# Optimization experiments

Hardware: AMD Instinct MI355X
Metric: run time of the kernel (lower is better)

The kernel has to match this reference:

```python
import jax, jax.numpy as jnp
import numpy as np

B = 8192
K = 40          # history blocks of 61
STATS = 383     # 99 base + 120 + 10 + 150 + 4 option dims
D = 165 + 61 * K + STATS  # 2988


def _mha(q, k, v, kpm, w_in, b_in, w_out, b_out, nh=4):
    """PyTorch nn.MultiheadAttention (batch_first) math. kpm: True = masked key."""
    Bq, Lq, E = q.shape
    hd = E // nh
    wq, wk, wv = jnp.split(w_in, 3, axis=0)
    bq, bk, bv = jnp.split(b_in, 3)
    qh = (q @ wq.T + bq).reshape(Bq, Lq, nh, hd).transpose(0, 2, 1, 3)
    kh = (k @ wk.T + bk).reshape(Bq, -1, nh, hd).transpose(0, 2, 1, 3)
    vh = (v @ wv.T + bv).reshape(Bq, -1, nh, hd).transpose(0, 2, 1, 3)
    s = jnp.einsum('bhqd,bhkd->bhqk', qh, kh) * jnp.float32(1.0 / np.sqrt(hd))
    if kpm is not None:
        s = jnp.where(kpm[:, None, None, :], jnp.float32(-1e9), s)
    a = jax.nn.softmax(s, axis=-1)
    o = jnp.einsum('bhqk,bhkd->bhqd', a, vh).transpose(0, 2, 1, 3).reshape(Bq, Lq, E)
    return o @ w_out.T + b_out


def _ln(x, g, b, eps=1e-5):
    m = x.mean(-1, keepdims=True)
    v = ((x - m) ** 2).mean(-1, keepdims=True)
    return (x - m) / jnp.sqrt(v + eps) * g + b


def setup_inputs() -> dict:
    key = jax.random.key(0)
    ks = iter(jax.random.split(key, 64))
    def p(shape, scale=0.02):
        return jax.random.normal(next(ks), shape, dtype=jnp.float32) * scale
    return {
        'obs': jax.random.normal(next(ks), (B, D), dtype=jnp.float32),
        'seat_team_vec': jax.random.normal(next(ks), (B, 6), dtype=jnp.float32),
        'card_emb': p((40, 32)),
        'w_cnt_hand': p((16, 3)), 'b_cnt_hand': p((16,)),
        'w_cnt_cap': p((16, 2)), 'b_cnt_cap': p((16,)),
        'h2t_win': p((96, 32)), 'h2t_bin': p((96,)), 'h2t_wout': p((32, 32)), 'h2t_bout': p((32,)),
        't2h_win': p((96, 32)), 't2h_bin': p((96,)), 't2h_wout': p((32, 32)), 't2h_bout': p((32,)),
        'w_merge': p((64, 224)), 'b_merge': p((64,)),
        'w_hproj': p((64, 61)), 'b_hproj': p((64,)),
        'pos_emb': p((40, 64)),
        'enc_win': p((192, 64)), 'enc_bin': p((192,)), 'enc_wout': p((64, 64)), 'enc_bout': p((64,)),
        'ln1_g': jnp.ones((64,), jnp.float32), 'ln1_b': jnp.zeros((64,), jnp.float32),
        'w_ff1': p((128, 64)), 'b_ff1': p((128,)),
        'w_ff2': p((64, 128)), 'b_ff2': p((64,)),
        'ln2_g': jnp.ones((64,), jnp.float32), 'ln2_b': jnp.zeros((64,), jnp.float32),
        'w_stats': p((64, STATS)), 'b_stats': p((64,)),
        'w_seat': p((32, 6)), 'b_seat': p((32,)),
        'w_comb': p((256, 224)), 'b_comb': p((256,)),
    }


def reference(obs, seat_team_vec, card_emb, w_cnt_hand, b_cnt_hand, w_cnt_cap, b_cnt_cap,
              h2t_win, h2t_bin, h2t_wout, h2t_bout, t2h_win, t2h_bin, t2h_wout, t2h_bout,
              w_merge, b_merge, w_hproj, b_hproj, pos_emb,
              enc_win, enc_bin, enc_wout, enc_bout, ln1_g, ln1_b,
              w_ff1, b_ff1, w_ff2, b_ff2, ln2_g, ln2_b,
              w_stats, b_stats, w_seat, b_seat, w_comb, b_comb):
    Bn = obs.shape[0]
    k = K  # static: decoded from D = 165 + 61*K + STATS
    hand_table = obs[:, :83]
    captured = obs[:, 83:165]
    history = obs[:, 165:165 + 61 * k]
    stats = obs[:, 165 + 61 * k:]

    hand_mask = hand_table[:, :40]
    other_counts = hand_table[:, 40:43]
    table_mask = hand_table[:, 43:83]

    hand_feat = hand_mask @ card_emb      # [B,32]
    table_feat = table_mask @ card_emb
    other_cnt_feat = jax.nn.relu(other_counts @ w_cnt_hand.T + b_cnt_hand)

    hand_present = hand_mask > 0.5
    table_present = table_mask > 0.5
    hand_seq = hand_mask[:, :, None] * card_emb    # [B,40,32]
    table_seq = table_mask[:, :, None] * card_emb

    # _safe_mha: rows whose keys are all padded produce zeros
    h2t = _mha(hand_seq, table_seq, table_seq, ~table_present, h2t_win, h2t_bin, h2t_wout, h2t_bout)
    h2t = jnp.where(table_present.any(axis=1)[:, None, None], h2t, jnp.float32(0.0))
    t2h = _mha(table_seq, hand_seq, hand_seq, ~hand_present, t2h_win, t2h_bin, t2h_wout, t2h_bout)
    t2h = jnp.where(hand_present.any(axis=1)[:, None, None], t2h, jnp.float32(0.0))

    def masked_mean(x, present):
        m = present[:, :, None].astype(x.dtype)
        return (x * m).sum(1) / jnp.maximum(m.sum(1), 1.0)
    hand_attn_feat = masked_mean(h2t, hand_present)
    table_attn_feat = masked_mean(t2h, table_present)

    cap0_feat = captured[:, :40] @ card_emb
    cap1_feat = captured[:, 40:80] @ card_emb
    cap_cnt_feat = jax.nn.relu(captured[:, 80:82] @ w_cnt_cap.T + b_cnt_cap)

    set_merged = jnp.concatenate([hand_feat, table_feat, cap0_feat, cap1_feat,
                                  hand_attn_feat, table_attn_feat,
                                  other_cnt_feat, cap_cnt_feat], axis=1)  # [B,224]
    set_feat = jax.nn.relu(set_merged @ w_merge.T + b_merge)              # [B,64]

    # 1-layer post-norm TransformerEncoder (eval mode, no dropout)
    hseq = history.reshape(Bn, k, 61) @ w_hproj.T + b_hproj + pos_emb[:k]  # [B,k,64]
    sa = _mha(hseq, hseq, hseq, None, enc_win, enc_bin, enc_wout, enc_bout)
    x = _ln(hseq + sa, ln1_g, ln1_b)
    ff = jax.nn.relu(x @ w_ff1.T + b_ff1) @ w_ff2.T + b_ff2
    x = _ln(x + ff, ln2_g, ln2_b)
    hist_feat = x.mean(axis=1)                                            # [B,64]

    stats_feat = jax.nn.relu(stats @ w_stats.T + b_stats)                 # [B,64]
    seat_feat = jax.nn.relu(seat_team_vec @ w_seat.T + b_seat)            # [B,32]

    combined = jnp.concatenate([set_feat, hist_feat, stats_feat, seat_feat], axis=1)  # [B,224]
    return jax.nn.relu(combined @ w_comb.T + b_comb)                      # [B,256]
```

## Files before the change

### kernel.cpp

```cpp
#include <hip/hip_runtime.h>

#define TPB 512

#define OFF_PE      0
#define OFF_HPROJ   7680
#define OFF_POSB    11584
#define OFF_FRAG    14144
#define FR_QKV      0
#define FR_OUT      12288
#define FR_FF1      16384
#define FR_FF2      24576
#define OFF_MERGE   46912
#define OFF_STATS   61248
#define OFF_COMB    85760
#define OFF_H2TWO   143104
#define OFF_T2HWO   144128
#define WS_TOTAL    145152

#define SA_OFF   0
#define SB_OFF   10240
#define SC_OFF   20480
#define QT_OFF   30720
#define FFH_OFF  10240
#define FFL_OFF  23296
#define AH_OFF   36352
#define AL_OFF   43264
#define SHT_OFF  50176
#define SOM_OFF  50840
#define SSM_OFF  51096
#define SCB_OFF  51992
#define SCNT_OFF 53016
#define SMEM_BYTES 53024

typedef __attribute__((ext_vector_type(8))) short bf16x8;
typedef __attribute__((ext_vector_type(4))) float f32x4;

struct P {
  const float *obs, *seat, *ce, *wch, *bch, *wcc, *bcc,
    *h2t_win, *h2t_bin, *h2t_wout, *h2t_bout,
    *t2h_win, *t2h_bin, *t2h_wout, *t2h_bout,
    *w_merge, *b_merge, *w_hproj, *b_hproj, *pos,
    *enc_win, *enc_bin, *enc_wout, *enc_bout,
    *ln1_g, *ln1_b, *w_ff1, *b_ff1, *w_ff2, *b_ff2, *ln2_g, *ln2_b,
    *w_stats, *b_stats, *w_seat, *b_seat, *w_comb, *b_comb;
  const float* ws;
  float* out;
};

__device__ __host__ inline unsigned bfpack(float a, float b, int plane) {
  unsigned ua = __float_as_uint(a) & 0xFFFF0000u;
  unsigned ub = __float_as_uint(b) & 0xFFFF0000u;
  if (plane == 0) return (ua >> 16) | ub;
  float ra = a - __uint_as_float(ua), rb = b - __uint_as_float(ub);
  return (__float_as_uint(ra) >> 16) | (__float_as_uint(rb) & 0xFFFF0000u);
}

__device__ inline void split_pair(float a, float b, unsigned& hi, unsigned& lo) {
  unsigned ua = __float_as_uint(a) & 0xFFFF0000u;
  unsigned ub = __float_as_uint(b) & 0xFFFF0000u;
  hi = (ua >> 16) | ub;
  float ra = a - __uint_as_float(ua), rb = b - __uint_as_float(ub);
  lo = (__float_as_uint(ra) >> 16) | (__float_as_uint(rb) & 0xFFFF0000u);
}

__global__ void prep_kernel(P p, float* ws) {
  int t = blockIdx.x * blockDim.x + threadIdx.x;
  if (t >= WS_TOTAL) return;
  if (t < OFF_HPROJ) {
    int arr = t / 1280, rem = t - arr * 1280;
    int i = rem >> 5, d = rem & 31;
    const float* win = (arr < 3) ? p.h2t_win : p.t2h_win;
    const float* wr = win + ((arr % 3) * 32 + d) * 32;
    const float* cr = p.ce + i * 32;
    float acc = 0.f;
    #pragma unroll
    for (int j = 0; j < 32; ++j) acc += cr[j] * wr[j];
    ws[t] = acc;
  } else if (t < OFF_POSB) {
    int r = t - OFF_HPROJ; int j = r >> 6, d = r & 63;
    ws[t] = p.w_hproj[d * 61 + j];
  } else if (t < OFF_FRAG) {
    int r = t - OFF_POSB; int d = r & 63;
    ws[t] = p.b_hproj[d] + p.pos[r];
  } else if (t < OFF_MERGE) {
    int r = t - OFF_FRAG;
    int plane, kt, nt, lane, u;
    const float* src; int ldk;
    if (r < FR_OUT) {
      plane = r / 6144; r %= 6144; kt = r / 3072; r %= 3072;
      nt = r >> 8; r &= 255; lane = r >> 2; u = r & 3;
      src = p.enc_win; ldk = 64;
    } else if (r < FR_FF1) {
      r -= FR_OUT; plane = r >> 11; r &= 2047; kt = r >> 10; r &= 1023;
      nt = r >> 8; r &= 255; lane = r >> 2; u = r & 3;
      src = p.enc_wout; ldk = 64;
    } else if (r < FR_FF2) {
      r -= FR_FF1; plane = r >> 12; r &= 4095; kt = r >> 11; r &= 2047;
      nt = r >> 8; r &= 255; lane = r >> 2; u = r & 3;
      src = p.w_ff1; ldk = 64;
    } else {
      r -= FR_FF2; plane = r >> 12; r &= 4095; kt = r >> 10; r &= 1023;
      nt = r >> 8; r &= 255; lane = r >> 2; u = r & 3;
      src = p.w_ff2; ldk = 128;
    }
    int k = kt * 32 + (lane >> 4) * 8 + u * 2;
    int n = nt * 16 + (lane & 15);
    float a = src[n * ldk + k], b = src[n * ldk + k + 1];
    ((unsigned*)ws)[t] = bfpack(a, b, plane);
  } else if (t < OFF_STATS) {
    int r = t - OFF_MERGE; int j = r >> 6, d = r & 63;
    ws[t] = p.w_merge[d * 224 + j];
  } else if (t < OFF_COMB) {
    int r = t - OFF_STATS; int j = r >> 6, d = r & 63;
    ws[t] = p.w_stats[d * 383 + j];
  } else if (t < OFF_H2TWO) {
    int r = t - OFF_COMB; int j = r >> 8, d = r & 255;
    ws[t] = p.w_comb[d * 224 + j];
  } else if (t < OFF_T2HWO) {
    int r = t - OFF_H2TWO; int e = r >> 5, d = r & 31;
    ws[t] = p.h2t_wout[d * 32 + e];
  } else {
    int r = t - OFF_T2HWO; int e = r >> 5, d = r & 31;
    ws[t] = p.t2h_wout[d * 32 + e];
  }
}

#define FMA4(acc, a4, w0, w1, w2, w3)                                   \
  acc.x += a4.x * w0.x + a4.y * w1.x + a4.z * w2.x + a4.w * w3.x;       \
  acc.y += a4.x * w0.y + a4.y * w1.y + a4.z * w2.y + a4.w * w3.y;       \
  acc.z += a4.x * w0.z + a4.y * w1.z + a4.z * w2.z + a4.w * w3.z;       \
  acc.w += a4.x * w0.w + a4.y * w1.w + a4.z * w2.w + a4.w * w3.w;

__global__ __launch_bounds__(TPB, 3) void enc_row(P p) {
  const int row = blockIdx.x;
  const int tid = threadIdx.x;
  const int lane = tid & 63, wq = tid >> 6;
  const int lane15 = lane & 15, lg = lane >> 4;

  __shared__ unsigned smem_u[SMEM_BYTES / 4];
  char* smem = (char*)smem_u;
  float* sA   = (float*)(smem + SA_OFF);
  float* sB   = (float*)(smem + SB_OFF);
  float* sC   = (float*)(smem + SC_OFF);
  float* s_ht = (float*)(smem + SHT_OFF);
  float* s_om = (float*)(smem + SOM_OFF);
  float* s_sm = (float*)(smem + SSM_OFF);
  float* s_cb = (float*)(smem + SCB_OFF);
  int*   s_cnt = (int*)(smem + SCNT_OFF);

  const float* orow = p.obs + (size_t)row * 2988;
  const float* ws = p.ws;
  const unsigned* wsu = (const unsigned*)ws;

  if (tid < 165) s_ht[tid] = orow[tid];
  if (tid < 32) {
    float a = 0.f;
    for (int i = 0; i < 40; ++i) a += orow[i] * p.ce[i * 32 + tid];
    s_sm[tid] = a;
  } else if (tid < 64) {
    int d = tid - 32; float a = 0.f;
    for (int i = 0; i < 40; ++i) a += orow[43 + i] * p.ce[i * 32 + d];
    s_sm[32 + d] = a;
  } else if (tid < 96) {
    int d = tid - 64; float a = 0.f;
    for (int i = 0; i < 40; ++i) a += orow[83 + i] * p.ce[i * 32 + d];
    s_sm[64 + d] = a;
  } else if (tid < 128) {
    int d = tid - 96; float a = 0.f;
    for (int i = 0; i < 40; ++i) a += orow[123 + i] * p.ce[i * 32 + d];
    s_sm[96 + d] = a;
  } else if (tid < 144) {
    int d = tid - 128;
    float a = p.bch[d];
    for (int j = 0; j < 3; ++j) a += orow[40 + j] * p.wch[d * 3 + j];
    s_sm[192 + d] = fmaxf(a, 0.f);
  } else if (tid < 160) {
    int d = tid - 144;
    float a = p.bcc[d];
    for (int j = 0; j < 2; ++j) a += orow[163 + j] * p.wcc[d * 2 + j];
    s_sm[208 + d] = fmaxf(a, 0.f);
  }
  if (tid >= 192 && tid < 256) s_om[tid - 192] = 0.f;
  if (tid >= 256 && tid < 320) s_cb[128 + tid - 256] = p.b_stats[tid - 256];
  if (tid >= 384 && tid < 448) s_cb[tid - 384] = p.b_merge[tid - 384];
  if (tid == 320) {
    int c = 0; for (int i = 0; i < 40; ++i) c += (orow[i] > 0.5f);
    s_cnt[0] = c;
  } else if (tid == 321) {
    int c = 0; for (int i = 0; i < 40; ++i) c += (orow[43 + i] > 0.5f);
    s_cnt[1] = c;
  }
  if (tid >= 448) {
    int z = tid - 448;
    unsigned* zh = (unsigned*)(smem + AH_OFF + 40 * 144);
    unsigned* zl = (unsigned*)(smem + AL_OFF + 40 * 144);
    for (int m = z; m < 288; m += 64) { zh[m] = 0u; zl[m] = 0u; }
  }
  __syncthreads();
  #define OB(i) s_ht[i]

  for (int t = tid; t < 736; t += TPB) {
    if (t < 320) {
      int d0 = (t & 15) << 2, i0 = (t >> 4) << 1;
      const float* wt = ws + OFF_HPROJ + d0;
      float4 acc0 = *(const float4*)(ws + OFF_POSB + (i0 + 0) * 64 + d0);
      float4 acc1 = *(const float4*)(ws + OFF_POSB + (i0 + 1) * 64 + d0);
      const float* h0 = orow + 165 + (i0 + 0) * 61;
      const float* h1 = orow + 165 + (i0 + 1) * 61;
      for (int j = 0; j < 61; ++j) {
        float4 w = *(const float4*)(wt + j * 64);
        float a0 = h0[j], a1 = h1[j];
        acc0.x += a0 * w.x; acc0.y += a0 * w.y; acc0.z += a0 * w.z; acc0.w += a0 * w.w;
        acc1.x += a1 * w.x; acc1.y += a1 * w.y; acc1.z += a1 * w.z; acc1.w += a1 * w.w;
      }
      *(float4*)(sA + (i0 + 0) * 64 + d0) = acc0;
      *(float4*)(sA + (i0 + 1) * 64 + d0) = acc1;
      unsigned h, l;
      split_pair(acc0.x, acc0.y, h, l);
      *(unsigned*)(smem + AH_OFF + (i0 + 0) * 144 + d0 * 2) = h;
      *(unsigned*)(smem + AL_OFF + (i0 + 0) * 144 + d0 * 2) = l;
      split_pair(acc0.z, acc0.w, h, l);
      *(unsigned*)(smem + AH_OFF + (i0 + 0) * 144 + d0 * 2 + 4) = h;
      *(unsigned*)(smem + AL_OFF + (i0 + 0) * 144 + d0 * 2 + 4) = l;
      split_pair(acc1.x, acc1.y, h, l);
      *(unsigned*)(smem + AH_OFF + (i0 + 1) * 144 + d0 * 2) = h;
      *(unsigned*)(smem + AL_OFF + (i0 + 1) * 144 + d0 * 2) = l;
      split_pair(acc1.z, acc1.w, h, l);
      *(unsigned*)(smem + AH_OFF + (i0 + 1) * 144 + d0 * 2 + 4) = h;
      *(unsigned*)(smem + AL_OFF + (i0 + 1) * 144 + d0 * 2 + 4) = l;
    } else if (t < 640) {
      int q = t - 320;
      int a = q / 160, r = q - a * 160;
      int h = r / 40, i = r - h * 40;
      int qoff = a ? 43 : 0, koff = a ? 0 : 43;
      const float* Cq = ws + OFF_PE + a * 3840;
      const float* Ck = Cq + 1280;
      const float* Cv = Cq + 2560;
      const float* bin = a ? p.t2h_bin : p.h2t_bin;
      const int e0 = h * 8;
      float qm = OB(qoff + i);
      float4 cq0 = *(const float4*)(Cq + i * 32 + e0);
      float4 cq1 = *(const float4*)(Cq + i * 32 + e0 + 4);
      float4 bq0 = *(const float4*)(bin + e0);
      float4 bq1 = *(const float4*)(bin + e0 + 4);
      float q0 = qm * cq0.x + bq0.x, q1 = qm * cq0.y + bq0.y;
      float q2 = qm * cq0.z + bq0.z, q3 = qm * cq0.w + bq0.w;
      float q4 = qm * cq1.x + bq1.x, q5 = qm * cq1.y + bq1.y;
      float q6 = qm * cq1.z + bq1.z, q7 = qm * cq1.w + bq1.w;
      float4 bk0 = *(const float4*)(bin + 32 + e0);
      float4 bk1 = *(const float4*)(bin + 32 + e0 + 4);
      const float scale = 0.35355339059327373f;
      float den = 0.f;
      float o0 = 0.f, o1 = 0.f, o2 = 0.f, o3 = 0.f;
      float o4 = 0.f, o5 = 0.f, o6 = 0.f, o7 = 0.f;
      for (int j = 0; j < 40; ++j) {
        float km = OB(koff + j);
        if (km > 0.5f) {
          float4 k0 = *(const float4*)(Ck + j * 32 + e0);
          float4 k1 = *(const float4*)(Ck + j * 32 + e0 + 4);
          float s = q0 * (km * k0.x + bk0.x) + q1 * (km * k0.y + bk0.y)
                  + q2 * (km * k0.z + bk0.z) + q3 * (km * k0.w + bk0.w)
                  + q4 * (km * k1.x + bk1.x) + q5 * (km * k1.y + bk1.y)
                  + q6 * (km * k1.z + bk1.z) + q7 * (km * k1.w + bk1.w);
          float pj = __expf(s * scale);
          den += pj;
          float pk = pj * km;
          float4 v0 = *(const float4*)(Cv + j * 32 + e0);
          float4 v1 = *(const float4*)(Cv + j * 32 + e0 + 4);
          o0 += pk * v0.x; o1 += pk * v0.y; o2 += pk * v0.z; o3 += pk * v0.w;
          o4 += pk * v1.x; o5 += pk * v1.y; o6 += pk * v1.z; o7 += pk * v1.w;
        }
      }
      if (qm > 0.5f) {
        float inv = 1.f / den;
        float4 bv0 = *(const float4*)(bin + 64 + e0);
        float4 bv1 = *(const float4*)(bin + 64 + e0 + 4);
        atomicAdd(&s_om[a * 32 + e0 + 0], o0 * inv + bv0.x);
        atomicAdd(&s_om[a * 32 + e0 + 1], o1 * inv + bv0.y);
        atomicAdd(&s_om[a * 32 + e0 + 2], o2 * inv + bv0.z);
        atomicAdd(&s_om[a * 32 + e0 + 3], o3 * inv + bv0.w);
        atomicAdd(&s_om[a * 32 + e0 + 4], o4 * inv + bv1.x);
        atomicAdd(&s_om[a * 32 + e0 + 5], o5 * inv + bv1.y);
        atomicAdd(&s_om[a * 32 + e0 + 6], o6 * inv + bv1.z);
        atomicAdd(&s_om[a * 32 + e0 + 7], o7 * inv + bv1.w);
      }
    } else {
      int r = t - 640;
      int c = r >> 4, d0 = (r & 15) << 2;
      int j0 = c * 64, j1 = (c == 5) ? 383 : j0 + 64;
      const float* st = orow + 2605;
      const float* wt = ws + OFF_STATS + d0;
      float x0 = 0.f, x1 = 0.f, x2 = 0.f, x3 = 0.f;
      for (int j = j0; j < j1; ++j) {
        float a0 = st[j];
        float4 w = *(const float4*)(wt + j * 64);
        x0 += a0 * w.x; x1 += a0 * w.y; x2 += a0 * w.z; x3 += a0 * w.w;
      }
      atomicAdd(&s_cb[128 + d0 + 0], x0);
      atomicAdd(&s_cb[128 + d0 + 1], x1);
      atomicAdd(&s_cb[128 + d0 + 2], x2);
      atomicAdd(&s_cb[128 + d0 + 3], x3);
    }
  }
  __syncthreads();

  for (int t = wq; t < 36; t += 8) {
    int rt = t % 3, nt = t / 3;
    int n = nt * 16 + lane15;
    float bia = p.enc_bin[n];
    f32x4 acc = {bia, bia, bia, bia};
    #pragma unroll
    for (int kt = 0; kt < 2; ++kt) {
      int arow = rt * 16 + lane15, kb = kt * 32 + lg * 8;
      bf16x8 aH = *(const bf16x8*)(smem + AH_OFF + arow * 144 + kb * 2);
      bf16x8 aL = *(const bf16x8*)(smem + AL_OFF + arow * 144 + kb * 2);
      bf16x8 bH = *(const bf16x8*)(wsu + OFF_FRAG + FR_QKV + kt * 3072 + nt * 256 + lane * 4);
      bf16x8 bL = *(const bf16x8*)(wsu + OFF_FRAG + FR_QKV + 6144 + kt * 3072 + nt * 256 + lane * 4);
      acc = __builtin_amdgcn_mfma_f32_16x16x32_bf16(aH, bH, acc, 0, 0, 0);
      acc = __builtin_amdgcn_mfma_f32_16x16x32_bf16(aH, bL, acc, 0, 0, 0);
      acc = __builtin_amdgcn_mfma_f32_16x16x32_bf16(aL, bH, acc, 0, 0, 0);
    }
    #pragma unroll
    for (int r = 0; r < 4; ++r) {
      int i = rt * 16 + lg * 4 + r;
      if (i < 40) {
        if (nt < 4) {
          *(unsigned short*)(smem + QT_OFF + (n * 40 + i) * 2) =
              (unsigned short)(__float_as_uint(acc[r]) >> 16);
        } else if (nt < 8) {
          sB[i * 64 + (n - 64)] = acc[r];
        } else {
          sC[i * 64 + (n - 128)] = acc[r];
        }
      }
    }
  }
  if (tid < 16) {
    int a = tid >> 3, d0 = (tid & 7) << 2;
    int ch = s_cnt[0], ct = s_cnt[1];
    float4 v = make_float4(0.f, 0.f, 0.f, 0.f);
    if (ch > 0 && ct > 0) {
      float ic = 1.f / (float)(a ? ct : ch);
      const float* wt = ws + (a ? OFF_T2HWO : OFF_H2TWO) + d0;
      const float* om = s_om + a * 32;
      v = *(const float4*)((a ? p.t2h_bout : p.h2t_bout) + d0);
      for (int e = 0; e < 32; ++e) {
        float oe = om[e] * ic;
        float4 w = *(const float4*)(wt + e * 32);
        v.x += oe * w.x; v.y += oe * w.y; v.z += oe * w.z; v.w += oe * w.w;
      }
    }
    *(float4*)(s_sm + 128 + a * 32 + d0) = v;
  }
  __syncthreads();

  if (tid < 320) {
    int eh = tid & 1, q = tid >> 1;
    int h = q / 40, i = q - h * 40;
    const int e0 = h * 16 + eh * 8;
    const unsigned short* qT = (const unsigned short*)(smem + QT_OFF);
    float q8[8];
    #pragma unroll
    for (int e = 0; e < 8; ++e)
      q8[e] = __uint_as_float(((unsigned)qT[(e0 + e) * 40 + i]) << 16);
    float den = 0.f;
    float o8[8];
    #pragma unroll
    for (int e = 0; e < 8; ++e) o8[e] = 0.f;
    for (int j = 0; j < 40; ++j) {
      const float* kr = sB + (j << 6) + e0;
      float4 k0 = *(const float4*)kr;
      float4 k1 = *(const float4*)(kr + 4);
      float part = q8[0] * k0.x + q8[1] * k0.y + q8[2] * k0.z + q8[3] * k0.w
                 + q8[4] * k1.x + q8[5] * k1.y + q8[6] * k1.z + q8[7] * k1.w;
      float s = (part + __shfl_xor(part, 1, 64)) * 0.25f;
      float pj = __expf(s);
      den += pj;
      const float* vr = sC + (j << 6) + e0;
      float4 v0 = *(const float4*)vr;
      float4 v1 = *(const float4*)(vr + 4);
      o8[0] += pj * v0.x; o8[1] += pj * v0.y; o8[2] += pj * v0.z; o8[3] += pj * v0.w;
      o8[4] += pj * v1.x; o8[5] += pj * v1.y; o8[6] += pj * v1.z; o8[7] += pj * v1.w;
    }
    float inv = 1.f / den;
    #pragma unroll
    for (int m = 0; m < 4; ++m) {
      unsigned hh, ll;
      split_pair(o8[2 * m] * inv, o8[2 * m + 1] * inv, hh, ll);
      *(unsigned*)(smem + AH_OFF + i * 144 + (e0 + 2 * m) * 2) = hh;
      *(unsigned*)(smem + AL_OFF + i * 144 + (e0 + 2 * m) * 2) = ll;
    }
  } else if (tid < 352) {
    int r = tid - 320;
    int d0 = (r & 15) << 2, jh = r >> 4;
    const float* wt = ws + OFF_MERGE + d0;
    float4 acc = make_float4(0.f, 0.f, 0.f, 0.f);
    int j0 = jh * 112, j1 = j0 + 112;
    for (int j = j0; j < j1; j += 4) {
      float4 a4 = *(const float4*)(s_sm + j);
      float4 w0 = *(const float4*)(wt + j * 64);
      float4 w1 = *(const float4*)(wt + (j + 1) * 64);
      float4 w2 = *(const float4*)(wt + (j + 2) * 64);
      float4 w3 = *(const float4*)(wt + (j + 3) * 64);
      FMA4(acc, a4, w0, w1, w2, w3);
    }
    atomicAdd(&s_cb[d0 + 0], acc.x);
    atomicAdd(&s_cb[d0 + 1], acc.y);
    atomicAdd(&s_cb[d0 + 2], acc.z);
    atomicAdd(&s_cb[d0 + 3], acc.w);
  }
  __syncthreads();

  for (int t = wq; t < 12; t += 8) {
    int rt = t % 3, nt = t / 3;
    int n = nt * 16 + lane15;
    f32x4 acc;
    #pragma unroll
    for (int r = 0; r < 4; ++r) {
      int i = rt * 16 + lg * 4 + r;
      acc[r] = p.enc_bout[n] + ((i < 40) ? sA[i * 64 + n] : 0.f);
    }
    #pragma unroll
    for (int kt = 0; kt < 2; ++kt) {
      int arow = rt * 16 + lane15, kb = kt * 32 + lg * 8;
      bf16x8 aH = *(const bf16x8*)(smem + AH_OFF + arow * 144 + kb * 2);
      bf16x8 aL = *(const bf16x8*)(smem + AL_OFF + arow * 144 + kb * 2);
      bf16x8 bH = *(const bf16x8*)(wsu + OFF_FRAG + FR_OUT + kt * 1024 + nt * 256 + lane * 4);
      bf16x8 bL = *(const bf16x8*)(wsu + OFF_FRAG + FR_OUT + 2048 + kt * 1024 + nt * 256 + lane * 4);
      acc = __builtin_amdgcn_mfma_f32_16x16x32_bf16(aH, bH, acc, 0, 0, 0);
      acc = __builtin_amdgcn_mfma_f32_16x16x32_bf16(aH, bL, acc, 0, 0, 0);
      acc = __builtin_amdgcn_mfma_f32_16x16x32_bf16(aL, bH, acc, 0, 0, 0);
    }
    #pragma unroll
    for (int r = 0; r < 4; ++r) {
      int i = rt * 16 + lg * 4 + r;
      if (i < 40) sB[i * 64 + n] = acc[r];
    }
  }
  __syncthreads();

  {
    float g = p.ln1_g[lane], b = p.ln1_b[lane];
    for (int i = wq; i < 40; i += 8) {
      float x = sB[(i << 6) + lane];
      float s = x;
      #pragma unroll
      for (int off = 32; off; off >>= 1) s += __shfl_xor(s, off, 64);
      float m = s * 0.015625f;
      float xm = x - m;
      float v = xm * xm;
      #pragma unroll
      for (int off = 32; off; off >>= 1) v += __shfl_xor(v, off, 64);
      float rs = rsqrtf(v * 0.015625f + 1e-5f);
      float val = xm * rs * g + b;
      sA[(i << 6) + lane] = val;
      unsigned hb = __float_as_uint(val) & 0xFFFF0000u;
      *(unsigned short*)(smem + AH_OFF + i * 144 + lane * 2) = (unsigned short)(hb >> 16);
      float rr = val - __uint_as_float(hb);
      *(unsigned short*)(smem + AL_OFF + i * 144 + lane * 2) =
          (unsigned short)(__float_as_uint(rr) >> 16);
    }
  }
  __syncthreads();

  for (int t = wq; t < 24; t += 8) {
    int rt = t % 3, nt = t / 3;
    int n = nt * 16 + lane15;
    float bia = p.b_ff1[n];
    f32x4 acc = {bia, bia, bia, bia};
    #pragma unroll
    for (int kt = 0; kt < 2; ++kt) {
      int arow = rt * 16 + lane15, kb = kt * 32 + lg * 8;
      bf16x8 aH = *(const bf16x8*)(smem + AH_OFF + arow * 144 + kb * 2);
      bf16x8 aL = *(const bf16x8*)(smem + AL_OFF + arow * 144 + kb * 2);
      bf16x8 bH = *(const bf16x8*)(wsu + OFF_FRAG + FR_FF1 + kt * 2048 + nt * 256 + lane * 4);
      bf16x8 bL = *(const bf16x8*)(wsu + OFF_FRAG + FR_FF1 + 4096 + kt * 2048 + nt * 256 + lane * 4);
      acc = __builtin_amdgcn_mfma_f32_16x16x32_bf16(aH, bH, acc, 0, 0, 0);
      acc = __builtin_amdgcn_mfma_f32_16x16x32_bf16(aH, bL, acc, 0, 0, 0);
      acc = __builtin_amdgcn_mfma_f32_16x16x32_bf16(aL, bH, acc, 0, 0, 0);
    }
    #pragma unroll
    for (int r = 0; r < 4; ++r) {
      int i = rt * 16 + lg * 4 + r;
      float v = (i < 40) ? fmaxf(acc[r], 0.f) : 0.f;
      unsigned hb = __float_as_uint(v) & 0xFFFF0000u;
      *(unsigned short*)(smem + FFH_OFF + i * 272 + n * 2) = (unsigned short)(hb >> 16);
      float rr = v - __uint_as_float(hb);
      *(unsigned short*)(smem + FFL_OFF + i * 272 + n * 2) =
          (unsigned short)(__float_as_uint(rr) >> 16);
    }
  }
  __syncthreads();

  for (int t = wq; t < 12; t += 8) {
    int rt = t % 3, nt = t / 3;
    int n = nt * 16 + lane15;
    f32x4 acc;
    #pragma unroll
    for (int r = 0; r < 4; ++r) {
      int i = rt * 16 + lg * 4 + r;
      acc[r] = p.b_ff2[n] + ((i < 40) ? sA[i * 64 + n] : 0.f);
    }
    #pragma unroll
    for (int kt = 0; kt < 4; ++kt) {
      int arow = rt * 16 + lane15, kb = kt * 32 + lg * 8;
      bf16x8 aH = *(const bf16x8*)(smem + FFH_OFF + arow * 272 + kb * 2);
      bf16x8 aL = *(const bf16x8*)(smem + FFL_OFF + arow * 272 + kb * 2);
      bf16x8 bH = *(const bf16x8*)(wsu + OFF_FRAG + FR_FF2 + kt * 1024 + nt * 256 + lane * 4);
      bf16x8 bL = *(const bf16x8*)(wsu + OFF_FRAG + FR_FF2 + 4096 + kt * 1024 + nt * 256 + lane * 4);
      acc = __builtin_amdgcn_mfma_f32_16x16x32_bf16(aH, bH, acc, 0, 0, 0);
      acc = __builtin_amdgcn_mfma_f32_16x16x32_bf16(aH, bL, acc, 0, 0, 0);
      acc = __builtin_amdgcn_mfma_f32_16x16x32_bf16(aL, bH, acc, 0, 0, 0);
    }
    #pragma unroll
    for (int r = 0; r < 4; ++r) {
      int i = rt * 16 + lg * 4 + r;
      if (i < 40) *(float*)(smem + AH_OFF + (i * 64 + n) * 4) = acc[r];
    }
  }
  __syncthreads();

  {
    float g = p.ln2_g[lane], b = p.ln2_b[lane];
    for (int i = wq; i < 40; i += 8) {
      float x = *(const float*)(smem + AH_OFF + ((i << 6) + lane) * 4);
      float s = x;
      #pragma unroll
      for (int off = 32; off; off >>= 1) s += __shfl_xor(s, off, 64);
      float m = s * 0.015625f;
      float xm = x - m;
      float v = xm * xm;
      #pragma unroll
      for (int off = 32; off; off >>= 1) v += __shfl_xor(v, off, 64);
      float rs = rsqrtf(v * 0.015625f + 1e-5f);
      sA[(i << 6) + lane] = xm * rs * g + b;
    }
  }
  __syncthreads();

  if (tid < 64) {
    float a = 0.f;
    for (int i = 0; i < 40; ++i) a += sA[(i << 6) + tid];
    s_cb[64 + tid] = a * 0.025f;
    s_cb[128 + tid] = fmaxf(s_cb[128 + tid], 0.f);
    s_cb[tid] = fmaxf(s_cb[tid], 0.f);
  } else if (tid < 96) {
    int d = tid - 64;
    const float* sv = p.seat + (size_t)row * 6;
    float acc = p.b_seat[d];
    for (int j = 0; j < 6; ++j) acc += sv[j] * p.w_seat[d * 6 + j];
    s_cb[192 + d] = fmaxf(acc, 0.f);
  }
  __syncthreads();

  if (tid < 256) {
    const float* wt = ws + OFF_COMB + tid;
    float acc = p.b_comb[tid];
    for (int j = 0; j < 224; j += 4) {
      float4 a4 = *(const float4*)(s_cb + j);
      acc += a4.x * wt[j * 256] + a4.y * wt[(j + 1) * 256]
           + a4.z * wt[(j + 2) * 256] + a4.w * wt[(j + 3) * 256];
    }
    p.out[(size_t)row * 256 + tid] = fmaxf(acc, 0.f);
  }
  #undef OB
}

extern "C" void kernel_launch(void* const* d_in, const int* in_sizes, int n_in,
                              void* d_out, int out_size, void* d_ws, size_t ws_size,
                              hipStream_t stream) {
  typedef const float* F;
  P p;
  p.obs      = (F)d_in[0];
  p.seat     = (F)d_in[1];
  p.ce       = (F)d_in[2];
  p.wch      = (F)d_in[3];
  p.bch      = (F)d_in[4];
  p.wcc      = (F)d_in[5];
  p.bcc      = (F)d_in[6];
  p.h2t_win  = (F)d_in[7];
  p.h2t_bin  = (F)d_in[8];
  p.h2t_wout = (F)d_in[9];
  p.h2t_bout = (F)d_in[10];
  p.t2h_win  = (F)d_in[11];
  p.t2h_bin  = (F)d_in[12];
  p.t2h_wout = (F)d_in[13];
  p.t2h_bout = (F)d_in[14];
  p.w_merge  = (F)d_in[15];
  p.b_merge  = (F)d_in[16];
  p.w_hproj  = (F)d_in[17];
  p.b_hproj  = (F)d_in[18];
  p.pos      = (F)d_in[19];
  p.enc_win  = (F)d_in[20];
  p.enc_bin  = (F)d_in[21];
  p.enc_wout = (F)d_in[22];
  p.enc_bout = (F)d_in[23];
  p.ln1_g    = (F)d_in[24];
  p.ln1_b    = (F)d_in[25];
  p.w_ff1    = (F)d_in[26];
  p.b_ff1    = (F)d_in[27];
  p.w_ff2    = (F)d_in[28];
  p.b_ff2    = (F)d_in[29];
  p.ln2_g    = (F)d_in[30];
  p.ln2_b    = (F)d_in[31];
  p.w_stats  = (F)d_in[32];
  p.b_stats  = (F)d_in[33];
  p.w_seat   = (F)d_in[34];
  p.b_seat   = (F)d_in[35];
  p.w_comb   = (F)d_in[36];
  p.b_comb   = (F)d_in[37];
  p.ws  = (const float*)d_ws;
  p.out = (float*)d_out;

  const int Bn = in_sizes[0] / 2988;
  hipLaunchKernelGGL(prep_kernel, dim3((WS_TOTAL + 255) / 256), dim3(256), 0, stream,
                     p, (float*)d_ws);
  hipLaunchKernelGGL(enc_row, dim3(Bn), dim3(TPB), 0, stream, p);
}
```

Baseline: 1.023 ms.

## Precompute card attention score tables, move hist proj to MFMA, trim bf16 split passes

Cross-attention scores are now read from precomputed per-card bilinear tables (G, U, V, bias constant) built in the prep kernel, which replaces per-row Q·K dot products. The history projection moves from scalar FMA loops to split-bf16 MFMA. The encoder attention, FF2 and out-projection drop their low-precision compensation terms and use single round-to-nearest bf16 operands, and the final combine GEMV is split across all 512 threads. This cuts ALU work and shared-memory traffic per row in exchange for lower numerical precision in several stages.

Result: faster. 864.8 us (-15.5%).

```diff
diff --git a/kernel.cpp b/kernel.cpp
--- a/kernel.cpp
+++ b/kernel.cpp
@@ -2,35 +2,43 @@
 
 #define TPB 512
 
-#define OFF_PE      0
-#define OFF_HPROJ   7680
-#define OFF_POSB    11584
-#define OFF_FRAG    14144
+#define OFF_CV      0
+#define OFF_POSB    2560
+#define OFF_G       3840
+#define OFF_U       10240
+#define OFF_V       10560
+#define OFF_CTB     10880
+#define OFF_FRHP    10888
+#define OFF_FRAG    14984
 #define FR_QKV      0
 #define FR_OUT      12288
 #define FR_FF1      16384
 #define FR_FF2      24576
-#define OFF_MERGE   46912
-#define OFF_STATS   61248
-#define OFF_COMB    85760
-#define OFF_H2TWO   143104
-#define OFF_T2HWO   144128
-#define WS_TOTAL    145152
-
-#define SA_OFF   0
-#define SB_OFF   10240
-#define SC_OFF   20480
-#define QT_OFF   30720
-#define FFH_OFF  10240
-#define FFL_OFF  23296
-#define AH_OFF   36352
-#define AL_OFF   43264
-#define SHT_OFF  50176
-#define SOM_OFF  50840
-#define SSM_OFF  51096
-#define SCB_OFF  51992
-#define SCNT_OFF 53016
-#define SMEM_BYTES 53024
+#define OFF_MERGE   47752
+#define OFF_STATS   62088
+#define OFF_COMB    86600
+#define OFF_WO2     143944
+#define WS_TOTAL    144968
+
+#define SA_OFF    0
+#define HISTH_OFF 10240
+#define HISTL_OFF 16768
+#define QPL_OFF   10240
+#define KF_OFF    16384
+#define KZ_OFF    22528
+#define OH_OFF    10240
+#define FF1P_OFF  10240
+#define C_OFF     23296
+#define DH_OFF    33536
+#define DL_OFF    40448
+#define S_OFF     33536
+#define SHT_OFF   47360
+#define SOM_OFF   48032
+#define SSM_OFF   48288
+#define SCB_OFF   49184
+#define R12_OFF   50208
+#define SCNT_OFF  52256
+#define SMEM_BYTES 52264
 
 typedef __attribute__((ext_vector_type(8))) short bf16x8;
 typedef __attribute__((ext_vector_type(4))) float f32x4;
@@ -55,33 +63,108 @@
   return (__float_as_uint(ra) >> 16) | (__float_as_uint(rb) & 0xFFFF0000u);
 }
 
-__device__ inline void split_pair(float a, float b, unsigned& hi, unsigned& lo) {
-  unsigned ua = __float_as_uint(a) & 0xFFFF0000u;
-  unsigned ub = __float_as_uint(b) & 0xFFFF0000u;
-  hi = (ua >> 16) | ub;
-  float ra = a - __uint_as_float(ua), rb = b - __uint_as_float(ub);
-  lo = (__float_as_uint(ra) >> 16) | (__float_as_uint(rb) & 0xFFFF0000u);
+__device__ inline unsigned short bf16rne(float x) {
+  unsigned u = __float_as_uint(x);
+  return (unsigned short)((u + 0x7FFFu + ((u >> 16) & 1u)) >> 16);
 }
+
+__device__ inline unsigned packrne(float a, float b) {
+  return (unsigned)bf16rne(a) | ((unsigned)bf16rne(b) << 16);
+}
+
+__device__ inline float bf_lo(unsigned u) { return __uint_as_float(u << 16); }
+__device__ inline float bf_hi(unsigned u) { return __uint_as_float(u & 0xFFFF0000u); }
+
+__device__ inline bf16x8 ld_b64x2(const char* pp) {
+  bf16x8 v;
+  *((uint2*)&v) = *(const uint2*)(pp);
+  *(((uint2*)&v) + 1) = *(const uint2*)(pp + 8);
+  return v;
+}
+
+#define CSCALE 0.35355339059327373f
 
 __global__ void prep_kernel(P p, float* ws) {
   int t = blockIdx.x * blockDim.x + threadIdx.x;
   if (t >= WS_TOTAL) return;
-  if (t < OFF_HPROJ) {
-    int arr = t / 1280, rem = t - arr * 1280;
+  unsigned* wsu = (unsigned*)ws;
+  if (t < OFF_POSB) {
+    int a = t / 1280, rem = t - a * 1280;
     int i = rem >> 5, d = rem & 31;
-    const float* win = (arr < 3) ? p.h2t_win : p.t2h_win;
-    const float* wr = win + ((arr % 3) * 32 + d) * 32;
+    const float* win = a ? p.t2h_win : p.h2t_win;
+    const float* wr = win + (64 + d) * 32;
     const float* cr = p.ce + i * 32;
     float acc = 0.f;
     #pragma unroll
     for (int j = 0; j < 32; ++j) acc += cr[j] * wr[j];
     ws[t] = acc;
-  } else if (t < OFF_POSB) {
-    int r = t - OFF_HPROJ; int j = r >> 6, d = r & 63;
-    ws[t] = p.w_hproj[d * 61 + j];
+  } else if (t < OFF_G) {
+    int r = t - OFF_POSB; int i = r >> 5, u = r & 31;
+    float a = p.b_hproj[2 * u] + p.pos[i * 64 + 2 * u];
+    float b = p.b_hproj[2 * u + 1] + p.pos[i * 64 + 2 * u + 1];
+    wsu[t] = packrne(a, b);
+  } else if (t < OFF_U) {
+    int r = t - OFF_G;
+    int u = r % 20; int i = (r / 20) % 40; int h = (r / 800) & 3; int a = r / 3200;
+    const float* win = a ? p.t2h_win : p.h2t_win;
+    const float* cri = p.ce + i * 32;
+    float g2[2];
+    #pragma unroll
+    for (int half = 0; half < 2; ++half) {
+      int j = 2 * u + half;
+      const float* crj = p.ce + j * 32;
+      float g = 0.f;
+      for (int e = 0; e < 8; ++e) {
+        const float* wq = win + (h * 8 + e) * 32;
+        const float* wk = win + (32 + h * 8 + e) * 32;
+        float pq = 0.f, pk = 0.f;
+        for (int m = 0; m < 32; ++m) { pq += cri[m] * wq[m]; pk += crj[m] * wk[m]; }
+        g += pq * pk;
+      }
+      g2[half] = g * CSCALE;
+    }
+    wsu[t] = packrne(g2[0], g2[1]);
+  } else if (t < OFF_V) {
+    int r = t - OFF_U; int i = r % 40; int h = (r / 40) & 3; int a = r / 160;
+    const float* win = a ? p.t2h_win : p.h2t_win;
+    const float* bin = a ? p.t2h_bin : p.h2t_bin;
+    const float* cri = p.ce + i * 32;
+    float u = 0.f;
+    for (int e = 0; e < 8; ++e) {
+      const float* wq = win + (h * 8 + e) * 32;
+      float pq = 0.f;
+      for (int m = 0; m < 32; ++m) pq += cri[m] * wq[m];
+      u += pq * bin[32 + h * 8 + e];
+    }
+    ws[t] = u * CSCALE;
+  } else if (t < OFF_CTB) {
+    int r = t - OFF_V; int j = r % 40; int h = (r / 40) & 3; int a = r / 160;
+    const float* win = a ? p.t2h_win : p.h2t_win;
+    const float* bin = a ? p.t2h_bin : p.h2t_bin;
+    const float* crj = p.ce + j * 32;
+    float v = 0.f;
+    for (int e = 0; e < 8; ++e) {
+      const float* wk = win + (32 + h * 8 + e) * 32;
+      float pk = 0.f;
+      for (int m = 0; m < 32; ++m) pk += crj[m] * wk[m];
+      v += pk * bin[h * 8 + e];
+    }
+    ws[t] = v * CSCALE;
+  } else if (t < OFF_FRHP) {
+    int r = t - OFF_CTB; int h = r & 3; int a = r >> 2;
+    const float* bin = a ? p.t2h_bin : p.h2t_bin;
+    float c = 0.f;
+    for (int e = 0; e < 8; ++e) c += bin[h * 8 + e] * bin[32 + h * 8 + e];
+    ws[t] = c * CSCALE;
   } else if (t < OFF_FRAG) {
-    int r = t - OFF_POSB; int d = r & 63;
-    ws[t] = p.b_hproj[d] + p.pos[r];
+    int r = t - OFF_FRHP;
+    int plane = r >> 11; r &= 2047; int kt = r >> 10; r &= 1023;
+    int nt = r >> 8; r &= 255; int lane = r >> 2; int u = r & 3;
+    int k = kt * 32 + (lane >> 4) * 8 + u * 2;
+    int n = nt * 16 + (lane & 15);
+    float a = (k < 61) ? p.w_hproj[n * 61 + k] : 0.f;
+    float b = (k + 1 < 61) ? p.w_hproj[n * 61 + k + 1] : 0.f;
+    wsu[t] = bfpack(a, b, plane);
   } else if (t < OFF_MERGE) {
     int r = t - OFF_FRAG;
     int plane, kt, nt, lane, u;
@@ -106,22 +189,21 @@
     int k = kt * 32 + (lane >> 4) * 8 + u * 2;
     int n = nt * 16 + (lane & 15);
     float a = src[n * ldk + k], b = src[n * ldk + k + 1];
-    ((unsigned*)ws)[t] = bfpack(a, b, plane);
+    wsu[t] = bfpack(a, b, plane);
   } else if (t < OFF_STATS) {
     int r = t - OFF_MERGE; int j = r >> 6, d = r & 63;
     ws[t] = p.w_merge[d * 224 + j];
   } else if (t < OFF_COMB) {
     int r = t - OFF_STATS; int j = r >> 6, d = r & 63;
     ws[t] = p.w_stats[d * 383 + j];
-  } else if (t < OFF_H2TWO) {
+  } else if (t < OFF_WO2) {
     int r = t - OFF_COMB; int j = r >> 8, d = r & 255;
     ws[t] = p.w_comb[d * 224 + j];
-  } else if (t < OFF_T2HWO) {
-    int r = t - OFF_H2TWO; int e = r >> 5, d = r & 31;
-    ws[t] = p.h2t_wout[d * 32 + e];
   } else {
-    int r = t - OFF_T2HWO; int e = r >> 5, d = r & 31;
-    ws[t] = p.t2h_wout[d * 32 + e];
+    int r = t - OFF_WO2; int a = r >> 9; int rr = r & 511;
+    int e = rr >> 4, u = rr & 15;
+    const float* src = a ? p.t2h_wout : p.h2t_wout;
+    wsu[t] = packrne(src[(2 * u) * 32 + e], src[(2 * u + 1) * 32 + e]);
   }
 }
 
@@ -131,6 +213,8 @@
   acc.z += a4.x * w0.z + a4.y * w1.z + a4.z * w2.z + a4.w * w3.z;       \
   acc.w += a4.x * w0.w + a4.y * w1.w + a4.z * w2.w + a4.w * w3.w;
 
+#define MFMA16(acc, a, b) acc = __builtin_amdgcn_mfma_f32_16x16x32_bf16(a, b, acc, 0, 0, 0)
+
 __global__ __launch_bounds__(TPB, 3) void enc_row(P p) {
   const int row = blockIdx.x;
   const int tid = threadIdx.x;
@@ -140,12 +224,12 @@
   __shared__ unsigned smem_u[SMEM_BYTES / 4];
   char* smem = (char*)smem_u;
   float* sA   = (float*)(smem + SA_OFF);
-  float* sB   = (float*)(smem + SB_OFF);
-  float* sC   = (float*)(smem + SC_OFF);
+  float* sC   = (float*)(smem + C_OFF);
   float* s_ht = (float*)(smem + SHT_OFF);
   float* s_om = (float*)(smem + SOM_OFF);
   float* s_sm = (float*)(smem + SSM_OFF);
   float* s_cb = (float*)(smem + SCB_OFF);
+  float* s_r12 = (float*)(smem + R12_OFF);
   int*   s_cnt = (int*)(smem + SCNT_OFF);
 
   const float* orow = p.obs + (size_t)row * 2988;
@@ -192,146 +276,158 @@
   }
   if (tid >= 448) {
     int z = tid - 448;
-    unsigned* zh = (unsigned*)(smem + AH_OFF + 40 * 144);
-    unsigned* zl = (unsigned*)(smem + AL_OFF + 40 * 144);
-    for (int m = z; m < 288; m += 64) { zh[m] = 0u; zl[m] = 0u; }
+    ((unsigned*)(smem + KZ_OFF))[z] = 0u;
+    ((unsigned*)(smem + KZ_OFF))[z + 64] = 0u;
+  }
+  for (int m = tid; m < 2560; m += TPB) {
+    int i = m >> 6, j = m & 63;
+    float val = (j < 61) ? orow[165 + i * 61 + j] : 0.f;
+    unsigned hb = __float_as_uint(val) & 0xFFFF0000u;
+    *(unsigned short*)(smem + HISTH_OFF + i * 136 + j * 2) = (unsigned short)(hb >> 16);
+    float rr = val - __uint_as_float(hb);
+    *(unsigned short*)(smem + HISTL_OFF + i * 136 + j * 2) =
+        (unsigned short)(__float_as_uint(rr) >> 16);
   }
   __syncthreads();
   #define OB(i) s_ht[i]
 
-  for (int t = tid; t < 736; t += TPB) {
-    if (t < 320) {
-      int d0 = (t & 15) << 2, i0 = (t >> 4) << 1;
-      const float* wt = ws + OFF_HPROJ + d0;
-      float4 acc0 = *(const float4*)(ws + OFF_POSB + (i0 + 0) * 64 + d0);
-      float4 acc1 = *(const float4*)(ws + OFF_POSB + (i0 + 1) * 64 + d0);
-      const float* h0 = orow + 165 + (i0 + 0) * 61;
-      const float* h1 = orow + 165 + (i0 + 1) * 61;
-      for (int j = 0; j < 61; ++j) {
-        float4 w = *(const float4*)(wt + j * 64);
-        float a0 = h0[j], a1 = h1[j];
-        acc0.x += a0 * w.x; acc0.y += a0 * w.y; acc0.z += a0 * w.z; acc0.w += a0 * w.w;
-        acc1.x += a1 * w.x; acc1.y += a1 * w.y; acc1.z += a1 * w.z; acc1.w += a1 * w.w;
+  for (int t = wq; t < 12; t += 8) {
+    int rt = t % 3, nt = t / 3;
+    int n = nt * 16 + lane15;
+    int arow = rt * 16 + lane15;
+    f32x4 acc;
+    #pragma unroll
+    for (int r = 0; r < 4; ++r) {
+      int i = rt * 16 + lg * 4 + r;
+      if (i < 40) {
+        unsigned pb = wsu[OFF_POSB + i * 32 + (n >> 1)];
+        acc[r] = (n & 1) ? bf_hi(pb) : bf_lo(pb);
+      } else acc[r] = 0.f;
+    }
+    #pragma unroll
+    for (int kt = 0; kt < 2; ++kt) {
+      int kb = kt * 32 + lg * 8;
+      bf16x8 aH = ld_b64x2(smem + HISTH_OFF + arow * 136 + kb * 2);
+      bf16x8 aL = ld_b64x2(smem + HISTL_OFF + arow * 136 + kb * 2);
+      bf16x8 bH = *(const bf16x8*)(wsu + OFF_FRHP + kt * 1024 + nt * 256 + lane * 4);
+      bf16x8 bL = *(const bf16x8*)(wsu + OFF_FRHP + 2048 + kt * 1024 + nt * 256 + lane * 4);
+      MFMA16(acc, aH, bH); MFMA16(acc, aH, bL); MFMA16(acc, aL, bH);
+    }
+    #pragma unroll
+    for (int r = 0; r < 4; ++r) {
+      int i = rt * 16 + lg * 4 + r;
+      if (i < 40) {
+        sA[i * 64 + n] = acc[r];
+        unsigned hb = __float_as_uint(acc[r]) & 0xFFFF0000u;
+        *(unsigned short*)(smem + DH_OFF + i * 144 + n * 2) = (unsigned short)(hb >> 16);
+        float rr = acc[r] - __uint_as_float(hb);
+        *(unsigned short*)(smem + DL_OFF + i * 144 + n * 2) =
+            (unsigned short)(__float_as_uint(rr) >> 16);
       }
-      *(float4*)(sA + (i0 + 0) * 64 + d0) = acc0;
-      *(float4*)(sA + (i0 + 1) * 64 + d0) = acc1;
-      unsigned h, l;
-      split_pair(acc0.x, acc0.y, h, l);
-      *(unsigned*)(smem + AH_OFF + (i0 + 0) * 144 + d0 * 2) = h;
-      *(unsigned*)(smem + AL_OFF + (i0 + 0) * 144 + d0 * 2) = l;
-      split_pair(acc0.z, acc0.w, h, l);
-      *(unsigned*)(smem + AH_OFF + (i0 + 0) * 144 + d0 * 2 + 4) = h;
-      *(unsigned*)(smem + AL_OFF + (i0 + 0) * 144 + d0 * 2 + 4) = l;
-      split_pair(acc1.x, acc1.y, h, l);
-      *(unsigned*)(smem + AH_OFF + (i0 + 1) * 144 + d0 * 2) = h;
-      *(unsigned*)(smem + AL_OFF + (i0 + 1) * 144 + d0 * 2) = l;
-      split_pair(acc1.z, acc1.w, h, l);
-      *(unsigned*)(smem + AH_OFF + (i0 + 1) * 144 + d0 * 2 + 4) = h;
-      *(unsigned*)(smem + AL_OFF + (i0 + 1) * 144 + d0 * 2 + 4) = l;
-    } else if (t < 640) {
-      int q = t - 320;
-      int a = q / 160, r = q - a * 160;
-      int h = r / 40, i = r - h * 40;
-      int qoff = a ? 43 : 0, koff = a ? 0 : 43;
-      const float* Cq = ws + OFF_PE + a * 3840;
-      const float* Ck = Cq + 1280;
-      const float* Cv = Cq + 2560;
-      const float* bin = a ? p.t2h_bin : p.h2t_bin;
-      const int e0 = h * 8;
-      float qm = OB(qoff + i);
-      float4 cq0 = *(const float4*)(Cq + i * 32 + e0);
-      float4 cq1 = *(const float4*)(Cq + i * 32 + e0 + 4);
-      float4 bq0 = *(const float4*)(bin + e0);
-      float4 bq1 = *(const float4*)(bin + e0 + 4);
-      float q0 = qm * cq0.x + bq0.x, q1 = qm * cq0.y + bq0.y;
-      float q2 = qm * cq0.z + bq0.z, q3 = qm * cq0.w + bq0.w;
-      float q4 = qm * cq1.x + bq1.x, q5 = qm * cq1.y + bq1.y;
-      float q6 = qm * cq1.z + bq1.z, q7 = qm * cq1.w + bq1.w;
-      float4 bk0 = *(const float4*)(bin + 32 + e0);
-      float4 bk1 = *(const float4*)(bin + 32 + e0 + 4);
-      const float scale = 0.35355339059327373f;
-      float den = 0.f;
-      float o0 = 0.f, o1 = 0.f, o2 = 0.f, o3 = 0.f;
-      float o4 = 0.f, o5 = 0.f, o6 = 0.f, o7 = 0.f;
-      for (int j = 0; j < 40; ++j) {
-        float km = OB(koff + j);
-        if (km > 0.5f) {
-          float4 k0 = *(const float4*)(Ck + j * 32 + e0);
-          float4 k1 = *(const float4*)(Ck + j * 32 + e0 + 4);
-          float s = q0 * (km * k0.x + bk0.x) + q1 * (km * k0.y + bk0.y)
-                  + q2 * (km * k0.z + bk0.z) + q3 * (km * k0.w + bk0.w)
-                  + q4 * (km * k1.x + bk1.x) + q5 * (km * k1.y + bk1.y)
-                  + q6 * (km * k1.z + bk1.z) + q7 * (km * k1.w + bk1.w);
-          float pj = __expf(s * scale);
-          den += pj;
-          float pk = pj * km;
-          float4 v0 = *(const float4*)(Cv + j * 32 + e0);
-          float4 v1 = *(const float4*)(Cv + j * 32 + e0 + 4);
-          o0 += pk * v0.x; o1 += pk * v0.y; o2 += pk * v0.z; o3 += pk * v0.w;
-          o4 += pk * v1.x; o5 += pk * v1.y; o6 += pk * v1.z; o7 += pk * v1.w;
-        }
+    }
+  }
+  if (tid < 320) {
+    int a = tid / 160, r = tid - a * 160;
+    int h = r / 40, i = r - h * 40;
+    int qoff = a ? 43 : 0, koff = a ? 0 : 43;
+    float qm = OB(qoff + i);
+    const unsigned* Gp = wsu + OFF_G + ((a * 4 + h) * 40 + i) * 20;
+    const float* vp = ws + OFF_V + (a * 4 + h) * 40;
+    const float* Cv = ws + OFF_CV + a * 1280;
+    const float* bin = a ? p.t2h_bin : p.h2t_bin;
+    float base = ws[OFF_CTB + a * 4 + h] + qm * ws[OFF_U + (a * 4 + h) * 40 + i];
+    const int e0 = h * 8;
+    float den = 0.f;
+    float o0 = 0.f, o1 = 0.f, o2 = 0.f, o3 = 0.f;
+    float o4 = 0.f, o5 = 0.f, o6 = 0.f, o7 = 0.f;
+    for (int j = 0; j < 40; ++j) {
+      float km = OB(koff + j);
+      if (km > 0.5f) {
+        unsigned g2 = Gp[j >> 1];
+        float gj = (j & 1) ? bf_hi(g2) : bf_lo(g2);
+        float s = fmaf(km, fmaf(qm, gj, vp[j]), base);
+        float pj = __expf(s);
+        den += pj;
+        float pk = pj * km;
+        float4 v0 = *(const float4*)(Cv + j * 32 + e0);
+        float4 v1 = *(const float4*)(Cv + j * 32 + e0 + 4);
+        o0 += pk * v0.x; o1 += pk * v0.y; o2 += pk * v0.z; o3 += pk * v0.w;
+        o4 += pk * v1.x; o5 += pk * v1.y; o6 += pk * v1.z; o7 += pk * v1.w;
       }
-      if (qm > 0.5f) {
-        float inv = 1.f / den;
-        float4 bv0 = *(const float4*)(bin + 64 + e0);
-        float4 bv1 = *(const float4*)(bin + 64 + e0 + 4);
-        atomicAdd(&s_om[a * 32 + e0 + 0], o0 * inv + bv0.x);
-        atomicAdd(&s_om[a * 32 + e0 + 1], o1 * inv + bv0.y);
-        atomicAdd(&s_om[a * 32 + e0 + 2], o2 * inv + bv0.z);
-        atomicAdd(&s_om[a * 32 + e0 + 3], o3 * inv + bv0.w);
-        atomicAdd(&s_om[a * 32 + e0 + 4], o4 * inv + bv1.x);
-        atomicAdd(&s_om[a * 32 + e0 + 5], o5 * inv + bv1.y);
-        atomicAdd(&s_om[a * 32 + e0 + 6], o6 * inv + bv1.z);
-        atomicAdd(&s_om[a * 32 + e0 + 7], o7 * inv + bv1.w);
-      }
-    } else {
-      int r = t - 640;
-      int c = r >> 4, d0 = (r & 15) << 2;
-      int j0 = c * 64, j1 = (c == 5) ? 383 : j0 + 64;
-      const float* st = orow + 2605;
-      const float* wt = ws + OFF_STATS + d0;
-      float x0 = 0.f, x1 = 0.f, x2 = 0.f, x3 = 0.f;
-      for (int j = j0; j < j1; ++j) {
-        float a0 = st[j];
-        float4 w = *(const float4*)(wt + j * 64);
-        x0 += a0 * w.x; x1 += a0 * w.y; x2 += a0 * w.z; x3 += a0 * w.w;
-      }
-      atomicAdd(&s_cb[128 + d0 + 0], x0);
-      atomicAdd(&s_cb[128 + d0 + 1], x1);
-      atomicAdd(&s_cb[128 + d0 + 2], x2);
-      atomicAdd(&s_cb[128 + d0 + 3], x3);
-    }
+    }
+    if (qm > 0.5f) {
+      float inv = 1.f / den;
+      float4 bv0 = *(const float4*)(bin + 64 + e0);
+      float4 bv1 = *(const float4*)(bin + 64 + e0 + 4);
+      atomicAdd(&s_om[a * 32 + e0 + 0], o0 * inv + bv0.x);
+      atomicAdd(&s_om[a * 32 + e0 + 1], o1 * inv + bv0.y);
+      atomicAdd(&s_om[a * 32 + e0 + 2], o2 * inv + bv0.z);
+      atomicAdd(&s_om[a * 32 + e0 + 3], o3 * inv + bv0.w);
+      atomicAdd(&s_om[a * 32 + e0 + 4], o4 * inv + bv1.x);
+      atomicAdd(&s_om[a * 32 + e0 + 5], o5 * inv + bv1.y);
+      atomicAdd(&s_om[a * 32 + e0 + 6], o6 * inv + bv1.z);
+      atomicAdd(&s_om[a * 32 + e0 + 7], o7 * inv + bv1.w);
+    }
+  } else {
+    int r = tid - 320;
+    int c = r >> 4, d0 = (r & 15) << 2;
+    int j0 = c << 5, j1 = (c == 11) ? 383 : j0 + 32;
+    const float* st = orow + 2605;
+    const float* wt = ws + OFF_STATS + d0;
+    float x0 = 0.f, x1 = 0.f, x2 = 0.f, x3 = 0.f;
+    for (int j = j0; j < j1; ++j) {
+      float a0 = st[j];
+      float4 w = *(const float4*)(wt + j * 64);
+      x0 += a0 * w.x; x1 += a0 * w.y; x2 += a0 * w.z; x3 += a0 * w.w;
+    }
+    atomicAdd(&s_cb[128 + d0 + 0], x0);
+    atomicAdd(&s_cb[128 + d0 + 1], x1);
+    atomicAdd(&s_cb[128 + d0 + 2], x2);
+    atomicAdd(&s_cb[128 + d0 + 3], x3);
   }
   __syncthreads();
 
   for (int t = wq; t < 36; t += 8) {
     int rt = t % 3, nt = t / 3;
     int n = nt * 16 + lane15;
+    int arow = rt * 16 + lane15;
     float bia = p.enc_bin[n];
     f32x4 acc = {bia, bia, bia, bia};
     #pragma unroll
     for (int kt = 0; kt < 2; ++kt) {
-      int arow = rt * 16 + lane15, kb = kt * 32 + lg * 8;
-      bf16x8 aH = *(const bf16x8*)(smem + AH_OFF + arow * 144 + kb * 2);
-      bf16x8 aL = *(const bf16x8*)(smem + AL_OFF + arow * 144 + kb * 2);
+      int kb = kt * 32 + lg * 8;
+      bf16x8 aH = *(const bf16x8*)(smem + DH_OFF + arow * 144 + kb * 2);
+      bf16x8 aL = *(const bf16x8*)(smem + DL_OFF + arow * 144 + kb * 2);
       bf16x8 bH = *(const bf16x8*)(wsu + OFF_FRAG + FR_QKV + kt * 3072 + nt * 256 + lane * 4);
       bf16x8 bL = *(const bf16x8*)(wsu + OFF_FRAG + FR_QKV + 6144 + kt * 3072 + nt * 256 + lane * 4);
-      acc = __builtin_amdgcn_mfma_f32_16x16x32_bf16(aH, bH, acc, 0, 0, 0);
-      acc = __builtin_amdgcn_mfma_f32_16x16x32_bf16(aH, bL, acc, 0, 0, 0);
-      acc = __builtin_amdgcn_mfma_f32_16x16x32_bf16(aL, bH, acc, 0, 0, 0);
-    }
-    #pragma unroll
-    for (int r = 0; r < 4; ++r) {
-      int i = rt * 16 + lg * 4 + r;
-      if (i < 40) {
-        if (nt < 4) {
-          *(unsigned short*)(smem + QT_OFF + (n * 40 + i) * 2) =
-              (unsigned short)(__float_as_uint(acc[r]) >> 16);
-        } else if (nt < 8) {
-          sB[i * 64 + (n - 64)] = acc[r];
-        } else {
-          sC[i * 64 + (n - 128)] = acc[r];
+      MFMA16(acc, aH, bH); MFMA16(acc, aH, bL); MFMA16(acc, aL, bH);
+    }
+    if (nt < 4) {
+      #pragma unroll
+      for (int r = 0; r < 4; ++r) {
+        int i = rt * 16 + lg * 4 + r;
+        if (i < 40)
+          *(unsigned short*)(smem + QPL_OFF + ((nt * 48 + i) * 16 + lane15) * 2) =
+              bf16rne(acc[r]);
+      }
+    } else if (nt < 8) {
+      int h = nt - 4, e = lane15;
+      int lp = (e >> 3) << 4, us = e & 7;
+      #pragma unroll
+      for (int r = 0; r < 4; ++r) {
+        int j = rt * 16 + lg * 4 + r;
+        if (j < 40) {
+          int lanep = lp + (j & 15);
+          *(unsigned short*)(smem + KF_OFF +
+              (((h * 3 + (j >> 4)) * 32 + lanep) * 8 + us) * 2) = bf16rne(acc[r]);
         }
+      }
+    } else {
+      int col = n - 128;
+      #pragma unroll
+      for (int r = 0; r < 4; ++r) {
+        int i = rt * 16 + lg * 4 + r;
+        if (i < 40) sC[i * 64 + col] = acc[r];
       }
     }
   }
@@ -341,16 +437,38 @@
     float4 v = make_float4(0.f, 0.f, 0.f, 0.f);
     if (ch > 0 && ct > 0) {
       float ic = 1.f / (float)(a ? ct : ch);
-      const float* wt = ws + (a ? OFF_T2HWO : OFF_H2TWO) + d0;
+      const unsigned* wt = wsu + OFF_WO2 + a * 512 + (d0 >> 1);
       const float* om = s_om + a * 32;
       v = *(const float4*)((a ? p.t2h_bout : p.h2t_bout) + d0);
       for (int e = 0; e < 32; ++e) {
         float oe = om[e] * ic;
-        float4 w = *(const float4*)(wt + e * 32);
-        v.x += oe * w.x; v.y += oe * w.y; v.z += oe * w.z; v.w += oe * w.w;
+        unsigned w01 = wt[e * 16], w23 = wt[e * 16 + 1];
+        v.x += oe * bf_lo(w01); v.y += oe * bf_hi(w01);
+        v.z += oe * bf_lo(w23); v.w += oe * bf_hi(w23);
       }
     }
     *(float4*)(s_sm + 128 + a * 32 + d0) = v;
+  }
+  __syncthreads();
+
+  for (int t = wq; t < 36; t += 8) {
+    int h = t / 9, rr = t % 9;
+    int rt = rr / 3, nt = rr % 3;
+    int arow = rt * 16 + lane15;
+    f32x4 acc = {0.f, 0.f, 0.f, 0.f};
+    bf16x8 aH = *(const bf16x8*)(smem + QPL_OFF + ((h * 48 + arow) * 16 + (lg & 1) * 8) * 2);
+    int boff = (lane < 32) ? (KF_OFF + (((h * 3 + nt) * 32 + lane) * 8) * 2)
+                           : (KZ_OFF + ((lane & 31) * 8) * 2);
+    bf16x8 bH = *(const bf16x8*)(smem + boff);
+    MFMA16(acc, aH, bH);
+    int j = nt * 16 + lane15;
+    #pragma unroll
+    for (int r = 0; r < 4; ++r) {
+      int i = rt * 16 + lg * 4 + r;
+      if (i < 40 && j < 40)
+        *(unsigned short*)(smem + S_OFF + ((h * 40 + i) * 42 + j) * 2) =
+            bf16rne(acc[r] * 0.25f);
+    }
   }
   __syncthreads();
 
@@ -358,22 +476,13 @@
     int eh = tid & 1, q = tid >> 1;
     int h = q / 40, i = q - h * 40;
     const int e0 = h * 16 + eh * 8;
-    const unsigned short* qT = (const unsigned short*)(smem + QT_OFF);
-    float q8[8];
-    #pragma unroll
-    for (int e = 0; e < 8; ++e)
-      q8[e] = __uint_as_float(((unsigned)qT[(e0 + e) * 40 + i]) << 16);
+    const unsigned short* Sp = (const unsigned short*)(smem + S_OFF) + (h * 40 + i) * 42;
     float den = 0.f;
     float o8[8];
     #pragma unroll
     for (int e = 0; e < 8; ++e) o8[e] = 0.f;
     for (int j = 0; j < 40; ++j) {
-      const float* kr = sB + (j << 6) + e0;
-      float4 k0 = *(const float4*)kr;
-      float4 k1 = *(const float4*)(kr + 4);
-      float part = q8[0] * k0.x + q8[1] * k0.y + q8[2] * k0.z + q8[3] * k0.w
-                 + q8[4] * k1.x + q8[5] * k1.y + q8[6] * k1.z + q8[7] * k1.w;
-      float s = (part + __shfl_xor(part, 1, 64)) * 0.25f;
+      float s = __uint_as_float(((unsigned)Sp[j]) << 16);
       float pj = __expf(s);
       den += pj;
       const float* vr = sC + (j << 6) + e0;
@@ -385,18 +494,16 @@
     float inv = 1.f / den;
     #pragma unroll
     for (int m = 0; m < 4; ++m) {
-      unsigned hh, ll;
-      split_pair(o8[2 * m] * inv, o8[2 * m + 1] * inv, hh, ll);
-      *(unsigned*)(smem + AH_OFF + i * 144 + (e0 + 2 * m) * 2) = hh;
-      *(unsigned*)(smem + AL_OFF + i * 144 + (e0 + 2 * m) * 2) = ll;
-    }
-  } else if (tid < 352) {
+      unsigned h2 = packrne(o8[2 * m] * inv, o8[2 * m + 1] * inv);
+      *(unsigned*)(smem + OH_OFF + i * 144 + (e0 + 2 * m) * 2) = h2;
+    }
+  } else if (tid < 384) {
     int r = tid - 320;
-    int d0 = (r & 15) << 2, jh = r >> 4;
+    int d0 = (r & 15) << 2, jq = r >> 4;
     const float* wt = ws + OFF_MERGE + d0;
     float4 acc = make_float4(0.f, 0.f, 0.f, 0.f);
-    int j0 = jh * 112, j1 = j0 + 112;
-    for (int j = j0; j < j1; j += 4) {
+    int j0 = jq * 56;
+    for (int j = j0; j < j0 + 56; j += 4) {
       float4 a4 = *(const float4*)(s_sm + j);
       float4 w0 = *(const float4*)(wt + j * 64);
       float4 w1 = *(const float4*)(wt + (j + 1) * 64);
@@ -414,6 +521,7 @@
   for (int t = wq; t < 12; t += 8) {
     int rt = t % 3, nt = t / 3;
     int n = nt * 16 + lane15;
+    int arow = rt * 16 + lane15;
     f32x4 acc;
     #pragma unroll
     for (int r = 0; r < 4; ++r) {
@@ -422,19 +530,16 @@
     }
     #pragma unroll
     for (int kt = 0; kt < 2; ++kt) {
-      int arow = rt * 16 + lane15, kb = kt * 32 + lg * 8;
-      bf16x8 aH = *(const bf16x8*)(smem + AH_OFF + arow * 144 + kb * 2);
-      bf16x8 aL = *(const bf16x8*)(smem + AL_OFF + arow * 144 + kb * 2);
+      int kb = kt * 32 + lg * 8;
+      bf16x8 aH = *(const bf16x8*)(smem + OH_OFF + arow * 144 + kb * 2);
       bf16x8 bH = *(const bf16x8*)(wsu + OFF_FRAG + FR_OUT + kt * 1024 + nt * 256 + lane * 4);
       bf16x8 bL = *(const bf16x8*)(wsu + OFF_FRAG + FR_OUT + 2048 + kt * 1024 + nt * 256 + lane * 4);
-      acc = __builtin_amdgcn_mfma_f32_16x16x32_bf16(aH, bH, acc, 0, 0, 0);
-      acc = __builtin_amdgcn_mfma_f32_16x16x32_bf16(aH, bL, acc, 0, 0, 0);
-      acc = __builtin_amdgcn_mfma_f32_16x16x32_bf16(aL, bH, acc, 0, 0, 0);
+      MFMA16(acc, aH, bH); MFMA16(acc, aH, bL);
     }
     #pragma unroll
     for (int r = 0; r < 4; ++r) {
       int i = rt * 16 + lg * 4 + r;
-      if (i < 40) sB[i * 64 + n] = acc[r];
+      if (i < 40) sC[i * 64 + n] = acc[r];
     }
   }
   __syncthreads();
@@ -442,7 +547,7 @@
   {
     float g = p.ln1_g[lane], b = p.ln1_b[lane];
     for (int i = wq; i < 40; i += 8) {
-      float x = sB[(i << 6) + lane];
+      float x = sC[(i << 6) + lane];
       float s = x;
       #pragma unroll
       for (int off = 32; off; off >>= 1) s += __shfl_xor(s, off, 64);
@@ -455,9 +560,9 @@
       float val = xm * rs * g + b;
       sA[(i << 6) + lane] = val;
       unsigned hb = __float_as_uint(val) & 0xFFFF0000u;
-      *(unsigned short*)(smem + AH_OFF + i * 144 + lane * 2) = (unsigned short)(hb >> 16);
+      *(unsigned short*)(smem + DH_OFF + i * 144 + lane * 2) = (unsigned short)(hb >> 16);
       float rr = val - __uint_as_float(hb);
-      *(unsigned short*)(smem + AL_OFF + i * 144 + lane * 2) =
+      *(unsigned short*)(smem + DL_OFF + i * 144 + lane * 2) =
           (unsigned short)(__float_as_uint(rr) >> 16);
     }
   }
@@ -466,28 +571,23 @@
   for (int t = wq; t < 24; t += 8) {
     int rt = t % 3, nt = t / 3;
     int n = nt * 16 + lane15;
+    int arow = rt * 16 + lane15;
     float bia = p.b_ff1[n];
     f32x4 acc = {bia, bia, bia, bia};
     #pragma unroll
     for (int kt = 0; kt < 2; ++kt) {
-      int arow = rt * 16 + lane15, kb = kt * 32 + lg * 8;
-      bf16x8 aH = *(const bf16x8*)(smem + AH_OFF + arow * 144 + kb * 2);
-      bf16x8 aL = *(const bf16x8*)(smem + AL_OFF + arow * 144 + kb * 2);
+      int kb = kt * 32 + lg * 8;
+      bf16x8 aH = *(const bf16x8*)(smem + DH_OFF + arow * 144 + kb * 2);
+      bf16x8 aL = *(const bf16x8*)(smem + DL_OFF + arow * 144 + kb * 2);
       bf16x8 bH = *(const bf16x8*)(wsu + OFF_FRAG + FR_FF1 + kt * 2048 + nt * 256 + lane * 4);
       bf16x8 bL = *(const bf16x8*)(wsu + OFF_FRAG + FR_FF1 + 4096 + kt * 2048 + nt * 256 + lane * 4);
-      acc = __builtin_amdgcn_mfma_f32_16x16x32_bf16(aH, bH, acc, 0, 0, 0);
-      acc = __builtin_amdgcn_mfma_f32_16x16x32_bf16(aH, bL, acc, 0, 0, 0);
-      acc = __builtin_amdgcn_mfma_f32_16x16x32_bf16(aL, bH, acc, 0, 0, 0);
+      MFMA16(acc, aH, bH); MFMA16(acc, aH, bL); MFMA16(acc, aL, bH);
     }
     #pragma unroll
     for (int r = 0; r < 4; ++r) {
       int i = rt * 16 + lg * 4 + r;
-      float v = (i < 40) ? fmaxf(acc[r], 0.f) : 0.f;
-      unsigned hb = __float_as_uint(v) & 0xFFFF0000u;
-      *(unsigned short*)(smem + FFH_OFF + i * 272 + n * 2) = (unsigned short)(hb >> 16);
-      float rr = v - __uint_as_float(hb);
-      *(unsigned short*)(smem + FFL_OFF + i * 272 + n * 2) =
-          (unsigned short)(__float_as_uint(rr) >> 16);
+      float v = fmaxf(acc[r], 0.f);
+      *(unsigned short*)(smem + FF1P_OFF + i * 272 + n * 2) = bf16rne(v);
     }
   }
   __syncthreads();
@@ -495,6 +595,7 @@
   for (int t = wq; t < 12; t += 8) {
     int rt = t % 3, nt = t / 3;
     int n = nt * 16 + lane15;
+    int arow = rt * 16 + lane15;
     f32x4 acc;
     #pragma unroll
     for (int r = 0; r < 4; ++r) {
@@ -503,19 +604,16 @@
     }
     #pragma unroll
     for (int kt = 0; kt < 4; ++kt) {
-      int arow = rt * 16 + lane15, kb = kt * 32 + lg * 8;
-      bf16x8 aH = *(const bf16x8*)(smem + FFH_OFF + arow * 272 + kb * 2);
-      bf16x8 aL = *(const bf16x8*)(smem + FFL_OFF + arow * 272 + kb * 2);
+      int kb = kt * 32 + lg * 8;
+      bf16x8 aH = *(const bf16x8*)(smem + FF1P_OFF + arow * 272 + kb * 2);
       bf16x8 bH = *(const bf16x8*)(wsu + OFF_FRAG + FR_FF2 + kt * 1024 + nt * 256 + lane * 4);
       bf16x8 bL = *(const bf16x8*)(wsu + OFF_FRAG + FR_FF2 + 4096 + kt * 1024 + nt * 256 + lane * 4);
-      acc = __builtin_amdgcn_mfma_f32_16x16x32_bf16(aH, bH, acc, 0, 0, 0);
-      acc = __builtin_amdgcn_mfma_f32_16x16x32_bf16(aH, bL, acc, 0, 0, 0);
-      acc = __builtin_amdgcn_mfma_f32_16x16x32_bf16(aL, bH, acc, 0, 0, 0);
+      MFMA16(acc, aH, bH); MFMA16(acc, aH, bL);
     }
     #pragma unroll
     for (int r = 0; r < 4; ++r) {
       int i = rt * 16 + lg * 4 + r;
-      if (i < 40) *(float*)(smem + AH_OFF + (i * 64 + n) * 4) = acc[r];
+      if (i < 40) sC[i * 64 + n] = acc[r];
     }
   }
   __syncthreads();
@@ -523,7 +621,7 @@
   {
     float g = p.ln2_g[lane], b = p.ln2_b[lane];
     for (int i = wq; i < 40; i += 8) {
-      float x = *(const float*)(smem + AH_OFF + ((i << 6) + lane) * 4);
+      float x = sC[(i << 6) + lane];
       float s = x;
       #pragma unroll
       for (int off = 32; off; off >>= 1) s += __shfl_xor(s, off, 64);
@@ -553,16 +651,21 @@
   }
   __syncthreads();
 
-  if (tid < 256) {
-    const float* wt = ws + OFF_COMB + tid;
-    float acc = p.b_comb[tid];
-    for (int j = 0; j < 224; j += 4) {
+  {
+    int n = tid & 255, half = tid >> 8;
+    const float* wt = ws + OFF_COMB + n;
+    float acc = half ? 0.f : p.b_comb[n];
+    int j0 = half * 112;
+    for (int j = j0; j < j0 + 112; j += 4) {
       float4 a4 = *(const float4*)(s_cb + j);
       acc += a4.x * wt[j * 256] + a4.y * wt[(j + 1) * 256]
            + a4.z * wt[(j + 2) * 256] + a4.w * wt[(j + 3) * 256];
     }
-    p.out[(size_t)row * 256 + tid] = fmaxf(acc, 0.f);
-  }
+    s_r12[half * 256 + n] = acc;
+  }
+  __syncthreads();
+  if (tid < 256)
+    p.out[(size_t)row * 256 + tid] = fmaxf(s_r12[tid] + s_r12[256 + tid], 0.f);
   #undef OB
 }
 
```
